# Kernel optimization log

Hardware: AMD Instinct MI355X
Metric: run time of the kernel (lower is better)

The kernel has to match this reference:

```python
import jax, jax.numpy as jnp
import numpy as np

D_MODEL = 2048
N_HEADS = 16
N_KV_HEADS = 4
HEAD_DIM = D_MODEL // N_HEADS  # 128
N_REP = N_HEADS // N_KV_HEADS  # 4
ROPE_BASE = 10000.0


def _rope_tables(T, head_dim, dtype):
    inv_freq = 1.0 / (ROPE_BASE ** (jnp.arange(0, head_dim, 2, dtype=jnp.float32) / head_dim))
    t = jnp.arange(T, dtype=jnp.float32)
    freqs = jnp.outer(t, inv_freq)               # [T, hd/2]
    emb = jnp.concatenate([freqs, freqs], axis=-1)  # [T, hd]
    return jnp.cos(emb).astype(dtype), jnp.sin(emb).astype(dtype)


def _rotate_half(x):
    x1, x2 = jnp.split(x, 2, axis=-1)
    return jnp.concatenate([-x2, x1], axis=-1)


def _apply_rope(x, cos, sin):
    # x: [B, H, T, hd]; cos/sin: [T, hd]
    return x * cos[None, None] + _rotate_half(x) * sin[None, None]


def setup_inputs() -> dict:
    key = jax.random.key(0)
    ks = jax.random.split(key, 5)
    B, T = 2, 2048
    s_in = 1.0 / np.sqrt(D_MODEL)
    return {
        "x": jax.random.normal(ks[0], (B, T, D_MODEL), jnp.float32),
        "Wq": jax.random.normal(ks[1], (D_MODEL, D_MODEL), jnp.float32) * s_in,
        "Wk": jax.random.normal(ks[2], (D_MODEL, N_KV_HEADS * HEAD_DIM), jnp.float32) * s_in,
        "Wv": jax.random.normal(ks[3], (D_MODEL, N_KV_HEADS * HEAD_DIM), jnp.float32) * s_in,
        "Wo": jax.random.normal(ks[4], (D_MODEL, D_MODEL), jnp.float32) * s_in,
    }


def reference(x, Wq, Wk, Wv, Wo):
    B, T, C = x.shape
    scale = HEAD_DIM ** -0.5
    q = (x @ Wq).reshape(B, T, N_HEADS, HEAD_DIM).transpose(0, 2, 1, 3)     # [B,H,T,hd]
    k = (x @ Wk).reshape(B, T, N_KV_HEADS, HEAD_DIM).transpose(0, 2, 1, 3)  # [B,Hkv,T,hd]
    v = (x @ Wv).reshape(B, T, N_KV_HEADS, HEAD_DIM).transpose(0, 2, 1, 3)
    cos, sin = _rope_tables(T, HEAD_DIM, x.dtype)
    q = _apply_rope(q, cos, sin)
    k = _apply_rope(k, cos, sin)
    # GQA: group query heads; avoid materializing expanded K/V
    qg = q.reshape(B, N_KV_HEADS, N_REP, T, HEAD_DIM)
    scores = jnp.einsum('bgrtd,bgsd->bgrts', qg, k) * scale                 # [B,Hkv,rep,T,S]
    causal = jnp.tril(jnp.ones((T, T), dtype=bool))
    scores = jnp.where(causal[None, None, None], scores, jnp.finfo(scores.dtype).min)
    attn = jax.nn.softmax(scores, axis=-1)
    out = jnp.einsum('bgrts,bgsd->bgrtd', attn, v)                          # [B,Hkv,rep,T,hd]
    out = out.reshape(B, N_HEADS, T, HEAD_DIM).transpose(0, 2, 1, 3).reshape(B, T, C)
    return out @ Wo, k, v
```

## Files before the change

kernel.cpp:

```cpp
#include <hip/hip_runtime.h>
#include <hip/hip_bf16.h>
#include <type_traits>


typedef short  short8 __attribute__((ext_vector_type(8)));
typedef float  f32x4  __attribute__((ext_vector_type(4)));
typedef float  f32x16 __attribute__((ext_vector_type(16)));

#define AS1(p) ((__attribute__((address_space(1))) void*)(p))
#define AS3(p) ((__attribute__((address_space(3))) void*)(p))

static __device__ inline short bf_bits(float f) {
    __hip_bfloat16 h = __float2bfloat16(f);
    return *reinterpret_cast<short*>(&h);
}

__global__ void prep_kernel(
    const float* __restrict__ x,
    const float* __restrict__ Wq, const float* __restrict__ Wk,
    const float* __restrict__ Wv, const float* __restrict__ Wo,
    __hip_bfloat16* __restrict__ xb,
    __hip_bfloat16* __restrict__ WqkvT, __hip_bfloat16* __restrict__ WoT)
{
    const int nb = blockIdx.x;
    const int tx = threadIdx.x, ty = threadIdx.y;
    if (nb >= 160) {
        int bid2 = (nb - 160) * 64 + blockIdx.y;
        int i = (bid2 * 256 + ty * 32 + tx) * 4;
        float4 v = *reinterpret_cast<const float4*>(x + i);
        ushort4 o;
        o.x = (unsigned short)bf_bits(v.x);
        o.y = (unsigned short)bf_bits(v.y);
        o.z = (unsigned short)bf_bits(v.z);
        o.w = (unsigned short)bf_bits(v.w);
        *reinterpret_cast<ushort4*>(reinterpret_cast<unsigned short*>(xb) + i) = o;
        return;
    }
    __shared__ float tile[32][33];
    const int k0 = blockIdx.y * 32;
    const float* W; int srcN, sn0, drow; __hip_bfloat16* dst;
    if (nb < 64) {
        int blk = nb & 3;
        int blk2 = ((blk & 1) << 1) | (blk >> 1);
        W = Wq; srcN = 2048; sn0 = nb * 32;
        dst = WqkvT; drow = ((nb >> 2) * 4 + blk2) * 32;
    } else if (nb < 80) {
        int i = nb - 64, blk = i & 3;
        int blk2 = ((blk & 1) << 1) | (blk >> 1);
        W = Wk; srcN = 512; sn0 = i * 32;
        dst = WqkvT; drow = 2048 + ((i >> 2) * 4 + blk2) * 32;
    } else if (nb < 96) {
        int i = nb - 80;
        W = Wv; srcN = 512; sn0 = i * 32;
        dst = WqkvT; drow = 2560 + i * 32;
    } else {
        int i = nb - 96;
        W = Wo; srcN = 2048; sn0 = i * 32;
        dst = WoT; drow = i * 32;
    }
#pragma unroll
    for (int i = 0; i < 32; i += 8)
        tile[ty + i][tx] = W[(size_t)(k0 + ty + i) * srcN + sn0 + tx];
    __syncthreads();
#pragma unroll
    for (int i = 0; i < 32; i += 8)
        dst[(size_t)(drow + ty + i) * 2048 + k0 + tx] = __float2bfloat16(tile[tx][ty + i]);
}

static __device__ inline void xcd_decode(int bid, int M, int N, int& m0, int& n0)
{
    const int xcd = bid & 7;
    const int idx = bid >> 3;
    const int mpx = (M >> 7) >> 3;
    const int rem = idx % (mpx * 4);
    const int mb = xcd * mpx + rem % mpx;
    const int nb = (idx / (mpx * 4)) * 4 + rem / mpx;
    m0 = mb << 7;
    n0 = nb << 7;
}

#define WAITV4 asm volatile("s_waitcnt vmcnt(4)" ::: "memory")
#define WAITV0 asm volatile("s_waitcnt vmcnt(0)" ::: "memory")

template <typename CT>
__global__ __launch_bounds__(256) void gemm_bt_kernel(
    const __hip_bfloat16* __restrict__ A,
    const __hip_bfloat16* __restrict__ BT,
    CT* __restrict__ C, int M, int N, int K)
{
    const int tid  = threadIdx.x;
    const int w    = tid >> 6;
    const int lane = tid & 63;
    const int l31  = lane & 31;
    const int hi   = lane >> 5;
    int m0, n0;
    xcd_decode(blockIdx.x, M, N, m0, n0);
    const int wm = (w >> 1) << 6;
    const int wn = (w & 1) << 6;

    __shared__ __hip_bfloat16 As[2][128 * 64];
    __shared__ __hip_bfloat16 Bs[2][128 * 64];

    f32x16 acc[2][2] = {};

#define GSTAGE(buf, k0_)                                                            \
    {                                                                               \
        _Pragma("unroll")                                                           \
        for (int i = 0; i < 4; ++i) {                                               \
            int c = tid + i * 256;                                                  \
            int row = c >> 3;                                                       \
            int soct = (c & 7) ^ (row & 7);                                         \
            const __hip_bfloat16* ga = A  + (size_t)(m0 + row) * K + (k0_) + soct * 8; \
            const __hip_bfloat16* gb = BT + (size_t)(n0 + row) * K + (k0_) + soct * 8; \
            __builtin_amdgcn_global_load_lds(AS1(ga), AS3(&As[buf][c * 8]), 16, 0, 0); \
            __builtin_amdgcn_global_load_lds(AS1(gb), AS3(&Bs[buf][c * 8]), 16, 0, 0); \
        }                                                                           \
    }

    GSTAGE(0, 0);
    __syncthreads();
    int cur = 0;
    const int nk = K >> 6;

    for (int t = 0; t < nk; ++t) {
        if (t + 1 < nk) GSTAGE(cur ^ 1, (t + 1) << 6);

        __builtin_amdgcn_s_setprio(1);
#pragma unroll
        for (int ks = 0; ks < 4; ++ks) {
            const int oct = ((ks * 2 + hi) ^ (l31 & 7)) << 3;
            short8 a[2], b[2];
#pragma unroll
            for (int mi = 0; mi < 2; ++mi)
                a[mi] = *reinterpret_cast<const short8*>(
                    reinterpret_cast<const short*>(&As[cur][0]) + (wm + mi * 32 + l31) * 64 + oct);
#pragma unroll
            for (int ni = 0; ni < 2; ++ni)
                b[ni] = *reinterpret_cast<const short8*>(
                    reinterpret_cast<const short*>(&Bs[cur][0]) + (wn + ni * 32 + l31) * 64 + oct);
#pragma unroll
            for (int mi = 0; mi < 2; ++mi)
#pragma unroll
                for (int ni = 0; ni < 2; ++ni)
                    acc[mi][ni] = __builtin_amdgcn_mfma_f32_32x32x16_bf16(
                        a[mi], b[ni], acc[mi][ni], 0, 0, 0);
        }
        __builtin_amdgcn_s_setprio(0);
        __syncthreads();
        cur ^= 1;
    }
#undef GSTAGE

#pragma unroll
    for (int mi = 0; mi < 2; ++mi)
#pragma unroll
        for (int ni = 0; ni < 2; ++ni)
#pragma unroll
            for (int reg = 0; reg < 16; ++reg) {
                int row = m0 + wm + mi * 32 + (reg & 3) + 8 * (reg >> 2) + 4 * hi;
                int col = n0 + wn + ni * 32 + l31;
                float v = acc[mi][ni][reg];
                if constexpr (std::is_same<CT, float>::value)
                    C[(size_t)row * N + col] = v;
                else
                    C[(size_t)row * N + col] = __float2bfloat16(v);
            }
}

__global__ __launch_bounds__(256) void gemm_qkv_fused(
    const __hip_bfloat16* __restrict__ A,
    const __hip_bfloat16* __restrict__ BT,
    __hip_bfloat16* __restrict__ qkv,
    float* __restrict__ outk,
    float* __restrict__ outv,
    __hip_bfloat16* __restrict__ VT)
{
    const int tid  = threadIdx.x;
    const int w    = tid >> 6;
    const int lane = tid & 63;
    const int l31  = lane & 31;
    const int hi   = lane >> 5;
    int m0, n0;
    xcd_decode(blockIdx.x, 4096, 3072, m0, n0);
    const int wm = (w >> 1) << 6;
    const int wn = (w & 1) << 6;
    const int K = 2048;

    __shared__ __hip_bfloat16 As[3][128 * 32];
    __shared__ __hip_bfloat16 Bs[3][128 * 32];

    f32x16 acc[2][2] = {};

#define GSTAGE(buf, k0_)                                                             \
    {                                                                                \
        _Pragma("unroll")                                                            \
        for (int i = 0; i < 2; ++i) {                                                \
            int c = tid + i * 256;                                                   \
            int row = c >> 2;                                                        \
            int soct = (c & 3) ^ ((row >> 1) & 3);                                   \
            const __hip_bfloat16* ga = A  + (size_t)(m0 + row) * K + (k0_) + soct * 8; \
            const __hip_bfloat16* gb = BT + (size_t)(n0 + row) * K + (k0_) + soct * 8; \
            __builtin_amdgcn_global_load_lds(AS1(ga), AS3(&As[buf][c * 8]), 16, 0, 0); \
            __builtin_amdgcn_global_load_lds(AS1(gb), AS3(&Bs[buf][c * 8]), 16, 0, 0); \
        }                                                                            \
    }

    const int nk = 64;
    GSTAGE(0, 0);
    GSTAGE(1, 32);
    int cur = 0, stg = 2;

    for (int t = 0; t < nk; ++t) {
        if (t == nk - 1) { WAITV0; } else { WAITV4; }
        __builtin_amdgcn_s_barrier();
        __builtin_amdgcn_sched_barrier(0);
        if (t + 2 < nk) GSTAGE(stg, (t + 2) << 5);

        __builtin_amdgcn_s_setprio(1);
#pragma unroll
        for (int ks = 0; ks < 2; ++ks) {
            short8 a[2], b[2];
#pragma unroll
            for (int mi = 0; mi < 2; ++mi) {
                int row = wm + mi * 32 + l31;
                a[mi] = *reinterpret_cast<const short8*>(
                    reinterpret_cast<const short*>(&As[cur][0])
                    + row * 32 + (((ks * 2 + hi) ^ ((row >> 1) & 3)) << 3));
            }
#pragma unroll
            for (int ni = 0; ni < 2; ++ni) {
                int row = wn + ni * 32 + l31;
                b[ni] = *reinterpret_cast<const short8*>(
                    reinterpret_cast<const short*>(&Bs[cur][0])
                    + row * 32 + (((ks * 2 + hi) ^ ((row >> 1) & 3)) << 3));
            }
#pragma unroll
            for (int mi = 0; mi < 2; ++mi)
#pragma unroll
                for (int ni = 0; ni < 2; ++ni)
                    acc[mi][ni] = __builtin_amdgcn_mfma_f32_32x32x16_bf16(
                        a[mi], b[ni], acc[mi][ni], 0, 0, 0);
        }
        __builtin_amdgcn_s_setprio(0);
        cur = (cur == 2) ? 0 : cur + 1;
        stg = (stg == 2) ? 0 : stg + 1;
    }
#undef GSTAGE

    const int hc = n0 >> 7;
    if (hc < 20) {
        const int c0 = wn + l31;
        const int d_lo = (wn ? 32 : 0) + l31;
        const float invf = exp2f((float)d_lo * -0.20762050593046f);
        const int kh = hc - 16;
#pragma unroll
        for (int mi = 0; mi < 2; ++mi)
#pragma unroll
            for (int reg = 0; reg < 16; ++reg) {
                int row = m0 + wm + mi * 32 + (reg & 3) + 8 * (reg >> 2) + 4 * hi;
                int b = row >> 11, t = row & 2047;
                float ang = (float)t * invf;
                float s = __sinf(ang), c = __cosf(ang);
                float x1 = acc[mi][0][reg], x2 = acc[mi][1][reg];
                float o1 = x1 * c - x2 * s;
                float o2 = x2 * c + x1 * s;
                __hip_bfloat16* q = qkv + (size_t)row * 3072 + hc * 128 + c0;
                q[0]  = __float2bfloat16(o1);
                q[32] = __float2bfloat16(o2);
                if (hc >= 16) {
                    float* ok = outk + (size_t)((b * 4 + kh) * 2048 + t) * 128 + d_lo;
                    ok[0]  = o1;
                    ok[64] = o2;
                }
            }
    } else {
        const int kh = hc - 20;
#pragma unroll
        for (int mi = 0; mi < 2; ++mi)
#pragma unroll
            for (int reg = 0; reg < 16; ++reg) {
                int row = m0 + wm + mi * 32 + (reg & 3) + 8 * (reg >> 2) + 4 * hi;
                int b = row >> 11, t = row & 2047;
#pragma unroll
                for (int ni = 0; ni < 2; ++ni) {
                    int d = wn + ni * 32 + l31;
                    float v = acc[mi][ni][reg];
                    outv[(size_t)((b * 4 + kh) * 2048 + t) * 128 + d] = v;
                    VT[(size_t)((b * 4 + kh) * 128 + d) * 2048 + t] = __float2bfloat16(v);
                }
            }
    }
}

__global__ __launch_bounds__(256, 2) void attn_kernel(
    const __hip_bfloat16* __restrict__ qkv,
    const __hip_bfloat16* __restrict__ VT,
    __hip_bfloat16* __restrict__ outO)
{
    const int bh = blockIdx.x;
    const int b = bh >> 4, h = bh & 15;
    const int kh = h >> 2;
    const int yb = blockIdx.y;
    const int qblk = (yb < 8) ? (15 - yb) : (yb - 8);
    const int tid = threadIdx.x;
    const int w = tid >> 6;
    const int lane = tid & 63;
    const int lo16 = lane & 15, grp = lane >> 4;
    const int qrow0 = qblk * 128 + w * 32;

    __shared__ short Ks[2][64 * 128];
    __shared__ short Vs[2][128 * 64];
    __shared__ short Ps[4][32 * 64];

    const short* qkvs = reinterpret_cast<const short*>(qkv);
    const size_t kbase = (size_t)b * 2048 * 3072 + 2048 + kh * 128;
    const short* vtb = reinterpret_cast<const short*>(VT) + (size_t)(b * 4 + kh) * 128 * 2048;
    short* pw = &Ps[w][0];

    short8 qf[2][4];
#pragma unroll
    for (int mi = 0; mi < 2; ++mi) {
        const short* qp = qkvs + (size_t)(b * 2048 + qrow0 + mi * 16 + lo16) * 3072
                        + h * 128 + grp * 8;
#pragma unroll
        for (int ss = 0; ss < 4; ++ss)
            qf[mi][ss] = *reinterpret_cast<const short8*>(qp + ss * 32);
    }

    f32x4 o[2][8] = {};
    f32x4 lac[2] = {};

    short8 ones;
#pragma unroll
    for (int jj = 0; jj < 8; ++jj) ones[jj] = (short)0x3F80;

    const float scl2 = 0.12752749545902973f;
    const int ntiles = qblk * 2 + 2;

#define STAGE(buf, kb_)                                                              \
    {                                                                                \
        _Pragma("unroll")                                                            \
        for (int i = 0; i < 4; ++i) {                                                \
            int c = tid + i * 256;                                                   \
            int row = c >> 4, c16 = (c & 15) ^ (row & 7);                            \
            const short* src = qkvs + kbase + (size_t)((kb_) + row) * 3072 + c16 * 8;\
            __builtin_amdgcn_global_load_lds(AS1(src),                               \
                AS3(&Ks[buf][(w * 64 + i * 256) * 8]), 16, 0, 0);                    \
        }                                                                            \
        _Pragma("unroll")                                                            \
        for (int i = 0; i < 4; ++i) {                                                \
            int c = tid + i * 256;                                                   \
            int d = c >> 3, c8 = (c & 7) ^ (d & 7);                                  \
            const short* src = vtb + (size_t)d * 2048 + (kb_) + c8 * 8;              \
            __builtin_amdgcn_global_load_lds(AS1(src),                               \
                AS3(&Vs[buf][(w * 64 + i * 256) * 8]), 16, 0, 0);                    \
        }                                                                            \
    }

    STAGE(0, 0);
    __syncthreads();
    int cur = 0;

    for (int t = 0; t < ntiles; ++t) {
        const int kb = t * 64;
        if (t + 1 < ntiles) STAGE(cur ^ 1, kb + 64);

        f32x4 sg[2][4];
        __builtin_amdgcn_s_setprio(1);
#pragma unroll
        for (int kg = 0; kg < 4; ++kg) {
            f32x4 a0 = {}, a1 = {};
#pragma unroll
            for (int ss = 0; ss < 4; ++ss) {
                short8 kf = *reinterpret_cast<const short8*>(
                    &Ks[cur][(kg * 16 + lo16) * 128 + (((ss * 4 + grp) ^ (lo16 & 7)) << 3)]);
                a0 = __builtin_amdgcn_mfma_f32_16x16x32_bf16(qf[0][ss], kf, a0, 0, 0, 0);
                a1 = __builtin_amdgcn_mfma_f32_16x16x32_bf16(qf[1][ss], kf, a1, 0, 0, 0);
            }
            sg[0][kg] = a0; sg[1][kg] = a1;
        }
        __builtin_amdgcn_s_setprio(0);

        if (kb + 63 > qrow0) {
#pragma unroll
            for (int mi = 0; mi < 2; ++mi)
#pragma unroll
                for (int kg = 0; kg < 4; ++kg) {
                    const int key = kb + kg * 16 + lo16;
#pragma unroll
                    for (int r = 0; r < 4; ++r) {
                        float v = sg[mi][kg][r] * scl2;
                        sg[mi][kg][r] = (key <= qrow0 + mi * 16 + grp * 4 + r) ? v : -1e30f;
                    }
                }
        } else {
#pragma unroll
            for (int mi = 0; mi < 2; ++mi)
#pragma unroll
                for (int kg = 0; kg < 4; ++kg)
#pragma unroll
                    for (int r = 0; r < 4; ++r) sg[mi][kg][r] *= scl2;
        }

#pragma unroll
        for (int mi = 0; mi < 2; ++mi)
#pragma unroll
            for (int kg = 0; kg < 4; ++kg)
#pragma unroll
                for (int r = 0; r < 4; ++r) {
                    float p = __builtin_amdgcn_exp2f(sg[mi][kg][r]);
                    int row = mi * 16 + grp * 4 + r;
                    int idx = row * 64 + (((kg * 2 + (lo16 >> 3)) ^ (row & 7)) << 3) + (lo16 & 7);
                    pw[idx] = bf_bits(p);
                }

        __builtin_amdgcn_s_setprio(1);
#pragma unroll
        for (int ks = 0; ks < 2; ++ks) {
            short8 pf0 = *reinterpret_cast<const short8*>(
                &pw[(0 * 16 + lo16) * 64 + (((ks * 4 + grp) ^ (lo16 & 7)) << 3)]);
            short8 pf1 = *reinterpret_cast<const short8*>(
                &pw[(1 * 16 + lo16) * 64 + (((ks * 4 + grp) ^ (lo16 & 7)) << 3)]);
            lac[0] = __builtin_amdgcn_mfma_f32_16x16x32_bf16(pf0, ones, lac[0], 0, 0, 0);
            lac[1] = __builtin_amdgcn_mfma_f32_16x16x32_bf16(pf1, ones, lac[1], 0, 0, 0);
#pragma unroll
            for (int jj = 0; jj < 8; ++jj) {
                short8 vf = *reinterpret_cast<const short8*>(
                    &Vs[cur][(jj * 16 + lo16) * 64 + (((ks * 4 + grp) ^ (lo16 & 7)) << 3)]);
                o[0][jj] = __builtin_amdgcn_mfma_f32_16x16x32_bf16(pf0, vf, o[0][jj], 0, 0, 0);
                o[1][jj] = __builtin_amdgcn_mfma_f32_16x16x32_bf16(pf1, vf, o[1][jj], 0, 0, 0);
            }
        }
        __builtin_amdgcn_s_setprio(0);

        __syncthreads();
        cur ^= 1;
    }
#undef STAGE

#pragma unroll
    for (int mi = 0; mi < 2; ++mi)
#pragma unroll
        for (int r = 0; r < 4; ++r) {
            float inv = 1.0f / lac[mi][r];
#pragma unroll
            for (int jj = 0; jj < 8; ++jj) {
                outO[(size_t)(b * 2048 + qrow0 + mi * 16 + grp * 4 + r) * 2048
                     + h * 128 + jj * 16 + lo16] = __float2bfloat16(o[mi][jj][r] * inv);
            }
        }
}

extern "C" void kernel_launch(void* const* d_in, const int* in_sizes, int n_in,
                              void* d_out, int out_size, void* d_ws, size_t ws_size,
                              hipStream_t stream)
{
    (void)in_sizes; (void)n_in; (void)out_size; (void)ws_size;
    const float* x  = (const float*)d_in[0];
    const float* Wq = (const float*)d_in[1];
    const float* Wk = (const float*)d_in[2];
    const float* Wv = (const float*)d_in[3];
    const float* Wo = (const float*)d_in[4];

    float* out0 = (float*)d_out;
    float* outk = out0 + 8388608;
    float* outv = out0 + 10485760;

    __hip_bfloat16* wsb    = (__hip_bfloat16*)d_ws;
    __hip_bfloat16* xb     = wsb;
    __hip_bfloat16* WqkvT  = xb + 8388608;
    __hip_bfloat16* WoT    = WqkvT + 6291456;
    __hip_bfloat16* qkv    = WoT + 4194304;
    __hip_bfloat16* VT     = qkv + 12582912;
    __hip_bfloat16* attn_o = xb;

    prep_kernel<<<dim3(288, 64), dim3(32, 8), 0, stream>>>(
        x, Wq, Wk, Wv, Wo, xb, WqkvT, WoT);

    gemm_qkv_fused<<<768, 256, 0, stream>>>(xb, WqkvT, qkv, outk, outv, VT);

    attn_kernel<<<dim3(32, 16), 256, 0, stream>>>(qkv, VT, attn_o);

    gemm_bt_kernel<float><<<512, 256, 0, stream>>>(attn_o, WoT, out0, 4096, 2048, 2048);
}
```

Before: 189.0 us.

## Switch attention to 32x32x16 MFMA with register-resident P via lane shuffles

Rewrites the attention inner loop to use 32x32x16 bf16 MFMAs. QK^T is computed transposed (K times Q), so each lane already holds score columns for its own query row. P is packed to bf16 and exchanged between wave halves with shuffles instead of a round trip through LDS. The row-sum is accumulated in scalar registers instead of through an MFMA against a ones vector. This removes the P shared-memory buffer, its LDS stores and loads, and the extra sum MFMAs, at the cost of more shuffles and a larger accumulator register footprint.

Measured after the change: 197.3 us. 4.4% more time.

```diff
diff --git a/kernel.cpp b/kernel.cpp
--- a/kernel.cpp
+++ b/kernel.cpp
@@ -13,6 +13,11 @@
 static __device__ inline short bf_bits(float f) {
     __hip_bfloat16 h = __float2bfloat16(f);
     return *reinterpret_cast<short*>(&h);
+}
+
+static __device__ inline unsigned pack2(float lo, float hi2) {
+    return (unsigned)(unsigned short)bf_bits(lo)
+         | ((unsigned)(unsigned short)bf_bits(hi2) << 16);
 }
 
 __global__ void prep_kernel(
@@ -305,34 +310,29 @@
     const int tid = threadIdx.x;
     const int w = tid >> 6;
     const int lane = tid & 63;
-    const int lo16 = lane & 15, grp = lane >> 4;
+    const int l31 = lane & 31;
+    const int hi = lane >> 5;
     const int qrow0 = qblk * 128 + w * 32;
+    const int qg = qrow0 + l31;
 
     __shared__ short Ks[2][64 * 128];
     __shared__ short Vs[2][128 * 64];
-    __shared__ short Ps[4][32 * 64];
+    __shared__ float Ls[4][32];
 
     const short* qkvs = reinterpret_cast<const short*>(qkv);
     const size_t kbase = (size_t)b * 2048 * 3072 + 2048 + kh * 128;
     const short* vtb = reinterpret_cast<const short*>(VT) + (size_t)(b * 4 + kh) * 128 * 2048;
-    short* pw = &Ps[w][0];
-
-    short8 qf[2][4];
-#pragma unroll
-    for (int mi = 0; mi < 2; ++mi) {
-        const short* qp = qkvs + (size_t)(b * 2048 + qrow0 + mi * 16 + lo16) * 3072
-                        + h * 128 + grp * 8;
-#pragma unroll
-        for (int ss = 0; ss < 4; ++ss)
-            qf[mi][ss] = *reinterpret_cast<const short8*>(qp + ss * 32);
-    }
-
-    f32x4 o[2][8] = {};
-    f32x4 lac[2] = {};
-
-    short8 ones;
-#pragma unroll
-    for (int jj = 0; jj < 8; ++jj) ones[jj] = (short)0x3F80;
+
+    short8 qf[8];
+    {
+        const short* qp = qkvs + (size_t)(b * 2048 + qg) * 3072 + h * 128 + hi * 8;
+#pragma unroll
+        for (int ss = 0; ss < 8; ++ss)
+            qf[ss] = *reinterpret_cast<const short8*>(qp + ss * 16);
+    }
+
+    f32x16 o[4] = {};
+    float lsum = 0.f;
 
     const float scl2 = 0.12752749545902973f;
     const int ntiles = qblk * 2 + 2;
@@ -357,6 +357,31 @@
         }                                                                            \
     }
 
+#define PVCHUNK(scv, kb2, ks2)                                                       \
+    {                                                                                \
+        unsigned pw0 = pack2((scv)[(ks2) * 8 + 0], (scv)[(ks2) * 8 + 1]);            \
+        unsigned pw1 = pack2((scv)[(ks2) * 8 + 2], (scv)[(ks2) * 8 + 3]);            \
+        unsigned pw2 = pack2((scv)[(ks2) * 8 + 4], (scv)[(ks2) * 8 + 5]);            \
+        unsigned pw3 = pack2((scv)[(ks2) * 8 + 6], (scv)[(ks2) * 8 + 7]);            \
+        unsigned s0 = (unsigned)__shfl_xor((int)pw0, 32);                            \
+        unsigned s1 = (unsigned)__shfl_xor((int)pw1, 32);                            \
+        unsigned s2 = (unsigned)__shfl_xor((int)pw2, 32);                            \
+        unsigned s3 = (unsigned)__shfl_xor((int)pw3, 32);                            \
+        int4 pi;                                                                     \
+        pi.x = (int)(hi ? s2 : pw0);                                                 \
+        pi.y = (int)(hi ? s3 : pw1);                                                 \
+        pi.z = (int)(hi ? pw2 : s0);                                                 \
+        pi.w = (int)(hi ? pw3 : s1);                                                 \
+        short8 pa = *reinterpret_cast<short8*>(&pi);                                 \
+        const int ob = (kb2) * 4 + (ks2) * 2 + hi;                                   \
+        _Pragma("unroll")                                                            \
+        for (int jb = 0; jb < 4; ++jb) {                                             \
+            short8 vf = *reinterpret_cast<const short8*>(                            \
+                &Vs[cur][(jb * 32 + l31) * 64 + ((ob ^ (l31 & 7)) << 3)]);           \
+            o[jb] = __builtin_amdgcn_mfma_f32_32x32x16_bf16(pa, vf, o[jb], 0, 0, 0); \
+        }                                                                            \
+    }
+
     STAGE(0, 0);
     __syncthreads();
     int cur = 0;
@@ -365,89 +390,67 @@
         const int kb = t * 64;
         if (t + 1 < ntiles) STAGE(cur ^ 1, kb + 64);
 
-        f32x4 sg[2][4];
+        f32x16 sc0 = {}, sc1 = {};
         __builtin_amdgcn_s_setprio(1);
 #pragma unroll
-        for (int kg = 0; kg < 4; ++kg) {
-            f32x4 a0 = {}, a1 = {};
-#pragma unroll
-            for (int ss = 0; ss < 4; ++ss) {
-                short8 kf = *reinterpret_cast<const short8*>(
-                    &Ks[cur][(kg * 16 + lo16) * 128 + (((ss * 4 + grp) ^ (lo16 & 7)) << 3)]);
-                a0 = __builtin_amdgcn_mfma_f32_16x16x32_bf16(qf[0][ss], kf, a0, 0, 0, 0);
-                a1 = __builtin_amdgcn_mfma_f32_16x16x32_bf16(qf[1][ss], kf, a1, 0, 0, 0);
-            }
-            sg[0][kg] = a0; sg[1][kg] = a1;
+        for (int ss = 0; ss < 8; ++ss) {
+            const int oct = ((ss * 2 + hi) ^ (l31 & 7)) << 3;
+            short8 k0 = *reinterpret_cast<const short8*>(&Ks[cur][l31 * 128 + oct]);
+            short8 k1 = *reinterpret_cast<const short8*>(&Ks[cur][(32 + l31) * 128 + oct]);
+            sc0 = __builtin_amdgcn_mfma_f32_32x32x16_bf16(k0, qf[ss], sc0, 0, 0, 0);
+            sc1 = __builtin_amdgcn_mfma_f32_32x32x16_bf16(k1, qf[ss], sc1, 0, 0, 0);
         }
         __builtin_amdgcn_s_setprio(0);
 
         if (kb + 63 > qrow0) {
 #pragma unroll
-            for (int mi = 0; mi < 2; ++mi)
-#pragma unroll
-                for (int kg = 0; kg < 4; ++kg) {
-                    const int key = kb + kg * 16 + lo16;
-#pragma unroll
-                    for (int r = 0; r < 4; ++r) {
-                        float v = sg[mi][kg][r] * scl2;
-                        sg[mi][kg][r] = (key <= qrow0 + mi * 16 + grp * 4 + r) ? v : -1e30f;
-                    }
-                }
+            for (int r = 0; r < 16; ++r) {
+                int kl = (r & 3) + 8 * (r >> 2) + 4 * hi;
+                float p0 = (kb + kl <= qg)
+                         ? __builtin_amdgcn_exp2f(sc0[r] * scl2) : 0.f;
+                float p1 = (kb + 32 + kl <= qg)
+                         ? __builtin_amdgcn_exp2f(sc1[r] * scl2) : 0.f;
+                sc0[r] = p0; sc1[r] = p1;
+                lsum += p0 + p1;
+            }
         } else {
 #pragma unroll
-            for (int mi = 0; mi < 2; ++mi)
-#pragma unroll
-                for (int kg = 0; kg < 4; ++kg)
-#pragma unroll
-                    for (int r = 0; r < 4; ++r) sg[mi][kg][r] *= scl2;
+            for (int r = 0; r < 16; ++r) {
+                float p0 = __builtin_amdgcn_exp2f(sc0[r] * scl2);
+                float p1 = __builtin_amdgcn_exp2f(sc1[r] * scl2);
+                sc0[r] = p0; sc1[r] = p1;
+                lsum += p0 + p1;
+            }
         }
 
-#pragma unroll
-        for (int mi = 0; mi < 2; ++mi)
-#pragma unroll
-            for (int kg = 0; kg < 4; ++kg)
-#pragma unroll
-                for (int r = 0; r < 4; ++r) {
-                    float p = __builtin_amdgcn_exp2f(sg[mi][kg][r]);
-                    int row = mi * 16 + grp * 4 + r;
-                    int idx = row * 64 + (((kg * 2 + (lo16 >> 3)) ^ (row & 7)) << 3) + (lo16 & 7);
-                    pw[idx] = bf_bits(p);
-                }
-
         __builtin_amdgcn_s_setprio(1);
-#pragma unroll
-        for (int ks = 0; ks < 2; ++ks) {
-            short8 pf0 = *reinterpret_cast<const short8*>(
-                &pw[(0 * 16 + lo16) * 64 + (((ks * 4 + grp) ^ (lo16 & 7)) << 3)]);
-            short8 pf1 = *reinterpret_cast<const short8*>(
-                &pw[(1 * 16 + lo16) * 64 + (((ks * 4 + grp) ^ (lo16 & 7)) << 3)]);
-            lac[0] = __builtin_amdgcn_mfma_f32_16x16x32_bf16(pf0, ones, lac[0], 0, 0, 0);
-            lac[1] = __builtin_amdgcn_mfma_f32_16x16x32_bf16(pf1, ones, lac[1], 0, 0, 0);
-#pragma unroll
-            for (int jj = 0; jj < 8; ++jj) {
-                short8 vf = *reinterpret_cast<const short8*>(
-                    &Vs[cur][(jj * 16 + lo16) * 64 + (((ks * 4 + grp) ^ (lo16 & 7)) << 3)]);
-                o[0][jj] = __builtin_amdgcn_mfma_f32_16x16x32_bf16(pf0, vf, o[0][jj], 0, 0, 0);
-                o[1][jj] = __builtin_amdgcn_mfma_f32_16x16x32_bf16(pf1, vf, o[1][jj], 0, 0, 0);
-            }
-        }
+        PVCHUNK(sc0, 0, 0);
+        PVCHUNK(sc0, 0, 1);
+        PVCHUNK(sc1, 1, 0);
+        PVCHUNK(sc1, 1, 1);
         __builtin_amdgcn_s_setprio(0);
 
         __syncthreads();
         cur ^= 1;
     }
 #undef STAGE
-
-#pragma unroll
-    for (int mi = 0; mi < 2; ++mi)
-#pragma unroll
-        for (int r = 0; r < 4; ++r) {
-            float inv = 1.0f / lac[mi][r];
-#pragma unroll
-            for (int jj = 0; jj < 8; ++jj) {
-                outO[(size_t)(b * 2048 + qrow0 + mi * 16 + grp * 4 + r) * 2048
-                     + h * 128 + jj * 16 + lo16] = __float2bfloat16(o[mi][jj][r] * inv);
-            }
+#undef PVCHUNK
+
+    float lt = lsum + __shfl_xor(lsum, 32);
+    if (hi == 0) Ls[w][l31] = 1.0f / lt;
+
+    float inv[16];
+#pragma unroll
+    for (int r = 0; r < 16; ++r)
+        inv[r] = Ls[w][(r & 3) + 8 * (r >> 2) + 4 * hi];
+
+#pragma unroll
+    for (int jb = 0; jb < 4; ++jb)
+#pragma unroll
+        for (int r = 0; r < 16; ++r) {
+            int qr = qrow0 + (r & 3) + 8 * (r >> 2) + 4 * hi;
+            outO[(size_t)(b * 2048 + qr) * 2048 + h * 128 + jb * 32 + l31] =
+                __float2bfloat16(o[jb][r] * inv[r]);
         }
 }
 
```
